# Optimization experiments

Measured on AMD Instinct MI355X. Metric: run time of the kernel, lower is better.

The kernel has to match this reference:

```python
import jax, jax.numpy as jnp
import numpy as np

NUM_NODES = 2048
NUM_OPS = 8
D, F, K = 64, 64, 64
H_NG = 128
H_EE = 64


def _make_edges(n):
    # edges[0]=i (src), edges[1]=j (dst) for i in [2,n), j in [0,i)
    src = np.concatenate([np.full(i, i, dtype=np.int64) for i in range(2, n)])
    dst = np.concatenate([np.arange(i, dtype=np.int64) for i in range(2, n)])
    return np.stack([src, dst])


def setup_inputs() -> dict:
    key = jax.random.key(0)
    ks = jax.random.split(key, 8)
    n = NUM_NODES
    s = lambda k, shape, fan_in: jax.random.normal(k, shape, jnp.float32) * (1.0 / np.sqrt(fan_in))
    return {
        "embed": jax.random.normal(ks[0], (n, D), jnp.float32),
        "W1": s(ks[1], (D, H_NG), D), "b1": jnp.zeros((H_NG,), jnp.float32),
        "W2": s(ks[2], (H_NG, H_NG), H_NG), "b2": jnp.zeros((H_NG,), jnp.float32),
        "W3": s(ks[3], (H_NG, F), H_NG), "b3": jnp.zeros((F,), jnp.float32),
        "We1": s(ks[4], (2 * F, H_EE), 2 * F), "be1": jnp.zeros((H_EE,), jnp.float32),
        "We2": s(ks[5], (H_EE, K), H_EE), "be2": jnp.zeros((K,), jnp.float32),
        "Wop": s(ks[6], (K, NUM_OPS), K), "bop": jnp.zeros((NUM_OPS,), jnp.float32),
        "edges": jnp.asarray(_make_edges(n)),
        "weights": jnp.ones((_make_edges(n).shape[1],), jnp.float32),
    }


def gcn_conv(x, W, b, src, dst, ew, n):
    # PyG GCNConv: x' = D^{-1/2} (A + I) D^{-1/2} (x W) + b, aggregated at dst
    h = x @ W
    loop = jnp.arange(n)
    src2 = jnp.concatenate([src, loop])
    dst2 = jnp.concatenate([dst, loop])
    w2 = jnp.concatenate([ew, jnp.ones((n,), x.dtype)])
    deg = jax.ops.segment_sum(w2, dst2, num_segments=n)
    dinv = jnp.where(deg > 0, jax.lax.rsqrt(deg), 0.0)
    norm = dinv[src2] * w2 * dinv[dst2]
    out = jax.ops.segment_sum(h[src2] * norm[:, None], dst2, num_segments=n)
    return out + b


def reference(embed, W1, b1, W2, b2, W3, b3, We1, be1, We2, be2, Wop, bop, edges, weights):
    n = embed.shape[0]
    src, dst = edges[0], edges[1]
    h = jax.nn.relu(gcn_conv(embed, W1, b1, src, dst, weights, n))
    h = jax.nn.relu(gcn_conv(h, W2, b2, src, dst, weights, n))
    h = jax.nn.relu(gcn_conv(h, W3, b3, src, dst, weights, n))  # [n, F]
    e = jnp.concatenate([h[src], h[dst]], axis=-1)              # [E, 2F]
    e = jax.nn.relu(e @ We1 + be1)
    e = jax.nn.relu(e @ We2 + be2)
    o = e @ Wop + bop                                            # [E, num_ops]
    p = jax.nn.softmax(o, axis=-1)
    # forward loop skips i == num_nodes-1; those rows of p remain zero
    mask = (src < n - 1)[:, None]
    return jnp.where(mask, p, 0.0)
```

## Files before the change

kernel.cpp:

```cpp
#include <hip/hip_runtime.h>
#include <math.h>

#define NN 2048
#define LASTN 2047

typedef __attribute__((ext_vector_type(8))) short short8;
typedef __attribute__((ext_vector_type(4))) float f32x4;
typedef __attribute__((ext_vector_type(4))) unsigned uint4v;

__device__ __forceinline__ float node_dinv(int j) {
  int deg = (j < 2) ? 2047 : (2048 - j);
  return rsqrtf((float)deg);
}

__device__ __forceinline__ void split_bf(float x, short& h, short& l) {
  unsigned u = __float_as_uint(x);
  unsigned r = u + 0x7FFFu + ((u >> 16) & 1u);
  h = (short)(r >> 16);
  float fh = __uint_as_float((r >> 16) << 16);
  float res = x - fh;
  unsigned u2 = __float_as_uint(res);
  unsigned r2 = u2 + 0x7FFFu + ((u2 >> 16) & 1u);
  l = (short)(r2 >> 16);
}

__device__ __forceinline__ unsigned cvt_pk_bf16(float a, float b) {
  unsigned r;
  asm("v_cvt_pk_bf16_f32 %0, %1, %2" : "=v"(r) : "v"(a), "v"(b));
  return r;
}

__device__ __forceinline__ void split_pair(float a, float b, unsigned& h, unsigned& l) {
  h = cvt_pk_bf16(a, b);
  float fa = __uint_as_float(h << 16);
  float fb = __uint_as_float(h & 0xFFFF0000u);
  l = cvt_pk_bf16(a - fa, b - fb);
}

__global__ __launch_bounds__(256) void prep(const float* __restrict__ embed,
                                            const float* __restrict__ We2,
                                            float* __restrict__ embedT,
                                            short* __restrict__ BfH,
                                            short* __restrict__ BfL) {
  __shared__ float tile[64][65];
  const int b = blockIdx.x;
  const int t = threadIdx.x;
  if (b < 32) {
    #pragma unroll
    for (int m = 0; m < 16; ++m) {
      int idx = m * 256 + t;
      int rl = idx >> 6, cc = idx & 63;
      tile[rl][cc] = embed[(b * 64 + rl) * 64 + cc];
    }
    __syncthreads();
    #pragma unroll
    for (int m = 0; m < 16; ++m) {
      int idx = m * 256 + t;
      int cc = idx >> 6, rl = idx & 63;
      embedT[cc * 2048 + b * 64 + rl] = tile[rl][cc];
    }
  } else {
    int tt = (b - 32) * 256 + t;
    int lane = tt & 63;
    int rest = tt >> 6;
    int ks = rest & 1;
    int ct = rest >> 1;
    int q = lane >> 4, l4 = lane & 15;
    int f = ct * 16 + l4;
    #pragma unroll
    for (int j = 0; j < 8; ++j) {
      int k = ks * 32 + q * 8 + j;
      float w = We2[k * 64 + f];
      short h, l;
      split_bf(w, h, l);
      int o = ((ct * 2 + ks) * 64 + lane) * 8 + j;
      BfH[o] = h;
      BfL[o] = l;
    }
  }
}

template <int K>
__global__ __launch_bounds__(512) void layer_fused(const float* __restrict__ XT,
                                                   const float* __restrict__ W,
                                                   const float* __restrict__ bias,
                                                   float* __restrict__ outT, int N) {
  const int c = blockIdx.x;
  const int t = threadIdx.x;
  __shared__ float wcol[K];
  __shared__ float sm[2048];
  __shared__ float part[512];
  if (t < K) wcol[t] = W[t * N + c];
  __syncthreads();
  float a0 = 0.f, a1 = 0.f, a2 = 0.f, a3 = 0.f;
  #pragma unroll 8
  for (int k = 0; k < K; ++k) {
    const float wk = wcol[k];
    const float* xr = XT + k * 2048 + t;
    a0 = fmaf(xr[0], wk, a0);
    a1 = fmaf(xr[512], wk, a1);
    a2 = fmaf(xr[1024], wk, a2);
    a3 = fmaf(xr[1536], wk, a3);
  }
  sm[t] = a0 * node_dinv(t);
  sm[t + 512] = a1 * node_dinv(t + 512);
  sm[t + 1024] = a2 * node_dinv(t + 1024);
  sm[t + 1536] = a3 * node_dinv(t + 1536);
  __syncthreads();
  const int j0 = 4 * t;
  float s0 = sm[j0], s1 = sm[j0 + 1], s2 = sm[j0 + 2], s3 = sm[j0 + 3];
  part[t] = (s0 + s1) + (s2 + s3);
  __syncthreads();
  for (int off = 1; off < 512; off <<= 1) {
    float v = part[t] + ((t + off < 512) ? part[t + off] : 0.f);
    __syncthreads();
    part[t] = v;
    __syncthreads();
  }
  float Q = (t < 511) ? part[t + 1] : 0.f;
  float Te3 = Q;
  float Te2 = Te3 + s3;
  float Te1 = Te2 + s2;
  float Te0 = Te1 + s1;
  const float bc = bias[c];
  float g0 = (j0 == 0) ? Te1 : Te0;
  float d0 = node_dinv(j0), d1 = node_dinv(j0 + 1);
  float d2 = node_dinv(j0 + 2), d3 = node_dinv(j0 + 3);
  float4 o;
  o.x = fmaxf(d0 * g0 + s0 * d0 + bc, 0.f);
  o.y = fmaxf(d1 * Te1 + s1 * d1 + bc, 0.f);
  o.z = fmaxf(d2 * Te2 + s2 * d2 + bc, 0.f);
  o.w = fmaxf(d3 * Te3 + s3 * d3 + bc, 0.f);
  *(float4*)(outT + (size_t)c * 2048 + j0) = o;
}

__global__ __launch_bounds__(256) void gemm_ab(const float* __restrict__ XT,
                                               const float* __restrict__ We1,
                                               const float* __restrict__ be1,
                                               float* __restrict__ A,
                                               float* __restrict__ B) {
  int idx = blockIdx.x * 256 + threadIdx.x;
  int r = idx >> 6, c = idx & 63;
  const float* WA = We1;
  const float* WB = We1 + 64 * 64;
  float a0 = 0.f, a1 = 0.f, b0 = 0.f, b1 = 0.f;
  for (int k = 0; k < 64; k += 2) {
    float x0 = XT[k * 2048 + r], x1 = XT[(k + 1) * 2048 + r];
    a0 = fmaf(x0, WA[k * 64 + c], a0);
    a1 = fmaf(x1, WA[(k + 1) * 64 + c], a1);
    b0 = fmaf(x0, WB[k * 64 + c], b0);
    b1 = fmaf(x1, WB[(k + 1) * 64 + c], b1);
  }
  A[idx] = a0 + a1 + be1[c];
  B[idx] = b0 + b1;
}

#define CHUNK 192
#define LSTR 196

__global__ __launch_bounds__(256, 3) void edge_mlp(const float* __restrict__ Amat,
                                                   const float* __restrict__ Bmat,
                                                   const short* __restrict__ BfH,
                                                   const short* __restrict__ BfL,
                                                   const float* __restrict__ be2,
                                                   const float* __restrict__ Wop,
                                                   const float* __restrict__ bop,
                                                   float* __restrict__ out) {
  const int i = LASTN - blockIdx.x;
  const long base = (long)i * (i - 1) / 2 - 1;
  const int tid = threadIdx.x;

  if (i == LASTN) {
    const float4 z = make_float4(0.f, 0.f, 0.f, 0.f);
    for (int j = blockIdx.y * 256 + tid; j < LASTN; j += gridDim.y * 256) {
      size_t off = ((size_t)(base + j)) * 8;
      *(float4*)(out + off) = z;
      *(float4*)(out + off + 4) = z;
    }
    return;
  }

  __shared__ __align__(16) float sm[64 * LSTR];

  const int l = tid & 63, w = tid >> 6;
  const int l4 = l & 15, q = l >> 4;

  const float4* Arow = (const float4*)(Amat + (size_t)i * 64);
  const float4 a00 = Arow[q * 2], a01 = Arow[q * 2 + 1];
  const float4 a10 = Arow[8 + q * 2], a11 = Arow[8 + q * 2 + 1];

  short8 Bh[8], Bl[8];
  #pragma unroll
  for (int u = 0; u < 8; ++u) {
    Bh[u] = *(const short8*)(BfH + (u * 64 + l) * 8);
    Bl[u] = *(const short8*)(BfL + (u * 64 + l) * 8);
  }

  #pragma unroll 1
  for (int cidx = blockIdx.y; cidx * CHUNK < i; cidx += gridDim.y) {
    const int j0 = cidx * CHUNK;

    #pragma unroll 1
    for (int mt = 0; mt < 3; ++mt) {
      const int mbase = (w * 3 + mt) * 16;
      int j = j0 + mbase + l4;
      int jc = min(j, i - 1);
      const float4* Brow = (const float4*)(Bmat + (size_t)jc * 64);

      short8 ah[2], al[2];
      #pragma unroll
      for (int ks = 0; ks < 2; ++ks) {
        float4 bb0 = Brow[ks * 8 + q * 2];
        float4 bb1 = Brow[ks * 8 + q * 2 + 1];
        float4 aa0 = ks ? a10 : a00;
        float4 aa1 = ks ? a11 : a01;
        float v0 = fmaxf(aa0.x + bb0.x, 0.f), v1 = fmaxf(aa0.y + bb0.y, 0.f);
        float v2 = fmaxf(aa0.z + bb0.z, 0.f), v3 = fmaxf(aa0.w + bb0.w, 0.f);
        float v4 = fmaxf(aa1.x + bb1.x, 0.f), v5 = fmaxf(aa1.y + bb1.y, 0.f);
        float v6 = fmaxf(aa1.z + bb1.z, 0.f), v7 = fmaxf(aa1.w + bb1.w, 0.f);
        unsigned h0, h1, h2, h3, L0, L1, L2, L3;
        split_pair(v0, v1, h0, L0);
        split_pair(v2, v3, h1, L1);
        split_pair(v4, v5, h2, L2);
        split_pair(v6, v7, h3, L3);
        ah[ks] = __builtin_bit_cast(short8, (uint4v){h0, h1, h2, h3});
        al[ks] = __builtin_bit_cast(short8, (uint4v){L0, L1, L2, L3});
      }

      f32x4 acc[4];
      #pragma unroll
      for (int ct = 0; ct < 4; ++ct) acc[ct] = (f32x4){0.f, 0.f, 0.f, 0.f};
      #pragma unroll
      for (int ct = 0; ct < 4; ++ct)
        acc[ct] = __builtin_amdgcn_mfma_f32_16x16x32_bf16(ah[0], Bh[ct * 2 + 0], acc[ct], 0, 0, 0);
      #pragma unroll
      for (int ct = 0; ct < 4; ++ct)
        acc[ct] = __builtin_amdgcn_mfma_f32_16x16x32_bf16(ah[1], Bh[ct * 2 + 1], acc[ct], 0, 0, 0);
      #pragma unroll
      for (int ct = 0; ct < 4; ++ct)
        acc[ct] = __builtin_amdgcn_mfma_f32_16x16x32_bf16(ah[0], Bl[ct * 2 + 0], acc[ct], 0, 0, 0);
      #pragma unroll
      for (int ct = 0; ct < 4; ++ct)
        acc[ct] = __builtin_amdgcn_mfma_f32_16x16x32_bf16(ah[1], Bl[ct * 2 + 1], acc[ct], 0, 0, 0);
      #pragma unroll
      for (int ct = 0; ct < 4; ++ct)
        acc[ct] = __builtin_amdgcn_mfma_f32_16x16x32_bf16(al[0], Bh[ct * 2 + 0], acc[ct], 0, 0, 0);
      #pragma unroll
      for (int ct = 0; ct < 4; ++ct)
        acc[ct] = __builtin_amdgcn_mfma_f32_16x16x32_bf16(al[1], Bh[ct * 2 + 1], acc[ct], 0, 0, 0);

      #pragma unroll
      for (int ct = 0; ct < 4; ++ct) {
        int f = ct * 16 + l4;
        float bias = be2[f];
        float4 st;
        st.x = fmaxf(acc[ct][0] + bias, 0.f);
        st.y = fmaxf(acc[ct][1] + bias, 0.f);
        st.z = fmaxf(acc[ct][2] + bias, 0.f);
        st.w = fmaxf(acc[ct][3] + bias, 0.f);
        *(float4*)(&sm[f * LSTR + mbase + q * 4]) = st;
      }
    }
    __syncthreads();

    if (tid < CHUNK) {
      int j = j0 + tid;
      if (j < i) {
        float o0 = bop[0], o1 = bop[1], o2 = bop[2], o3 = bop[3];
        float o4 = bop[4], o5 = bop[5], o6 = bop[6], o7 = bop[7];
        #pragma unroll 8
        for (int f = 0; f < 64; ++f) {
          float v = sm[f * LSTR + tid];
          o0 = fmaf(v, Wop[f * 8 + 0], o0);
          o1 = fmaf(v, Wop[f * 8 + 1], o1);
          o2 = fmaf(v, Wop[f * 8 + 2], o2);
          o3 = fmaf(v, Wop[f * 8 + 3], o3);
          o4 = fmaf(v, Wop[f * 8 + 4], o4);
          o5 = fmaf(v, Wop[f * 8 + 5], o5);
          o6 = fmaf(v, Wop[f * 8 + 6], o6);
          o7 = fmaf(v, Wop[f * 8 + 7], o7);
        }
        float mx = fmaxf(fmaxf(fmaxf(o0, o1), fmaxf(o2, o3)),
                         fmaxf(fmaxf(o4, o5), fmaxf(o6, o7)));
        float p0 = __expf(o0 - mx), p1 = __expf(o1 - mx), p2 = __expf(o2 - mx);
        float p3 = __expf(o3 - mx), p4 = __expf(o4 - mx), p5 = __expf(o5 - mx);
        float p6 = __expf(o6 - mx), p7 = __expf(o7 - mx);
        float rs = 1.0f / (((p0 + p1) + (p2 + p3)) + ((p4 + p5) + (p6 + p7)));
        size_t off = ((size_t)(base + j)) * 8;
        *(float4*)(out + off) = make_float4(p0 * rs, p1 * rs, p2 * rs, p3 * rs);
        *(float4*)(out + off + 4) = make_float4(p4 * rs, p5 * rs, p6 * rs, p7 * rs);
      }
    }
    __syncthreads();
  }
}

extern "C" void kernel_launch(void* const* d_in, const int* in_sizes, int n_in,
                              void* d_out, int out_size, void* d_ws, size_t ws_size,
                              hipStream_t stream) {
  const float* embed = (const float*)d_in[0];
  const float* W1 = (const float*)d_in[1];
  const float* b1 = (const float*)d_in[2];
  const float* W2 = (const float*)d_in[3];
  const float* b2 = (const float*)d_in[4];
  const float* W3 = (const float*)d_in[5];
  const float* b3 = (const float*)d_in[6];
  const float* We1 = (const float*)d_in[7];
  const float* be1 = (const float*)d_in[8];
  const float* We2 = (const float*)d_in[9];
  const float* be2 = (const float*)d_in[10];
  const float* Wop = (const float*)d_in[11];
  const float* bop = (const float*)d_in[12];

  float* ws = (float*)d_ws;
  float* embedT = ws;
  float* h2T = ws;
  float* h1T = ws + 262144;
  float* Abuf = ws + 262144;
  float* Bbuf = ws + 393216;
  float* h3T = ws + 524288;
  short* BfH = (short*)(ws + 655360);
  short* BfL = (short*)(ws + 657408);
  float* outp = (float*)d_out;

  prep<<<34, 256, 0, stream>>>(embed, We2, embedT, BfH, BfL);
  layer_fused<64><<<128, 512, 0, stream>>>(embedT, W1, b1, h1T, 128);
  layer_fused<128><<<128, 512, 0, stream>>>(h1T, W2, b2, h2T, 128);
  layer_fused<128><<<64, 512, 0, stream>>>(h2T, W3, b3, h3T, 64);
  gemm_ab<<<512, 256, 0, stream>>>(h3T, We1, be1, Abuf, Bbuf);

  dim3 ge(2046, 4, 1);
  edge_mlp<<<ge, 256, 0, stream>>>(Abuf, Bbuf, BfH, BfL, be2, Wop, bop, outp);
}
```

Measured before the change: 266.8 us.

## Double-buffer edge MLP chunks and overlap softmax epilogue with next MFMA stage

Shrinks the edge chunk to 64 rows and double-buffers the shared-memory hidden tile. One rotating wave runs the Wop projection and softmax on the current chunk while the other three waves compute the next chunk's MFMA tiles. This removes the phase where only some threads did the serial epilogue while the rest sat idle between barriers. It also halves the y-grid to 2, hoists the bias loads and raises the occupancy hint to 4. In exchange there are more barrier iterations per block and an uneven split of tiles across waves.

```diff
diff --git a/kernel.cpp b/kernel.cpp
--- a/kernel.cpp
+++ b/kernel.cpp
@@ -155,10 +155,11 @@
   B[idx] = b0 + b1;
 }
 
-#define CHUNK 192
-#define LSTR 196
-
-__global__ __launch_bounds__(256, 3) void edge_mlp(const float* __restrict__ Amat,
+#define CHUNK 64
+#define LSTR 68
+#define EGY 2
+
+__global__ __launch_bounds__(256, 4) void edge_mlp(const float* __restrict__ Amat,
                                                    const float* __restrict__ Bmat,
                                                    const short* __restrict__ BfH,
                                                    const short* __restrict__ BfL,
@@ -172,7 +173,7 @@
 
   if (i == LASTN) {
     const float4 z = make_float4(0.f, 0.f, 0.f, 0.f);
-    for (int j = blockIdx.y * 256 + tid; j < LASTN; j += gridDim.y * 256) {
+    for (int j = blockIdx.y * 256 + tid; j < LASTN; j += EGY * 256) {
       size_t off = ((size_t)(base + j)) * 8;
       *(float4*)(out + off) = z;
       *(float4*)(out + off + 4) = z;
@@ -180,7 +181,10 @@
     return;
   }
 
-  __shared__ __align__(16) float sm[64 * LSTR];
+  int c = blockIdx.y;
+  if (c * CHUNK >= i) return;
+
+  __shared__ __align__(16) float sm[2][64 * LSTR];
 
   const int l = tid & 63, w = tid >> 6;
   const int l4 = l & 15, q = l >> 4;
@@ -195,103 +199,122 @@
     Bh[u] = *(const short8*)(BfH + (u * 64 + l) * 8);
     Bl[u] = *(const short8*)(BfL + (u * 64 + l) * 8);
   }
-
-  #pragma unroll 1
-  for (int cidx = blockIdx.y; cidx * CHUNK < i; cidx += gridDim.y) {
-    const int j0 = cidx * CHUNK;
-
-    #pragma unroll 1
-    for (int mt = 0; mt < 3; ++mt) {
-      const int mbase = (w * 3 + mt) * 16;
-      int j = j0 + mbase + l4;
-      int jc = min(j, i - 1);
-      const float4* Brow = (const float4*)(Bmat + (size_t)jc * 64);
-
-      short8 ah[2], al[2];
-      #pragma unroll
-      for (int ks = 0; ks < 2; ++ks) {
-        float4 bb0 = Brow[ks * 8 + q * 2];
-        float4 bb1 = Brow[ks * 8 + q * 2 + 1];
-        float4 aa0 = ks ? a10 : a00;
-        float4 aa1 = ks ? a11 : a01;
-        float v0 = fmaxf(aa0.x + bb0.x, 0.f), v1 = fmaxf(aa0.y + bb0.y, 0.f);
-        float v2 = fmaxf(aa0.z + bb0.z, 0.f), v3 = fmaxf(aa0.w + bb0.w, 0.f);
-        float v4 = fmaxf(aa1.x + bb1.x, 0.f), v5 = fmaxf(aa1.y + bb1.y, 0.f);
-        float v6 = fmaxf(aa1.z + bb1.z, 0.f), v7 = fmaxf(aa1.w + bb1.w, 0.f);
-        unsigned h0, h1, h2, h3, L0, L1, L2, L3;
-        split_pair(v0, v1, h0, L0);
-        split_pair(v2, v3, h1, L1);
-        split_pair(v4, v5, h2, L2);
-        split_pair(v6, v7, h3, L3);
-        ah[ks] = __builtin_bit_cast(short8, (uint4v){h0, h1, h2, h3});
-        al[ks] = __builtin_bit_cast(short8, (uint4v){L0, L1, L2, L3});
+  float bias[4];
+  #pragma unroll
+  for (int ct = 0; ct < 4; ++ct) bias[ct] = be2[ct * 16 + l4];
+
+  auto stage_tile = [&](int cbase, int t, float* smb) {
+    int j = cbase + t * 16 + l4;
+    int jc = min(j, i - 1);
+    const float4* Brow = (const float4*)(Bmat + (size_t)jc * 64);
+
+    short8 ah[2], al[2];
+    #pragma unroll
+    for (int ks = 0; ks < 2; ++ks) {
+      float4 bb0 = Brow[ks * 8 + q * 2];
+      float4 bb1 = Brow[ks * 8 + q * 2 + 1];
+      float4 aa0 = ks ? a10 : a00;
+      float4 aa1 = ks ? a11 : a01;
+      float v0 = fmaxf(aa0.x + bb0.x, 0.f), v1 = fmaxf(aa0.y + bb0.y, 0.f);
+      float v2 = fmaxf(aa0.z + bb0.z, 0.f), v3 = fmaxf(aa0.w + bb0.w, 0.f);
+      float v4 = fmaxf(aa1.x + bb1.x, 0.f), v5 = fmaxf(aa1.y + bb1.y, 0.f);
+      float v6 = fmaxf(aa1.z + bb1.z, 0.f), v7 = fmaxf(aa1.w + bb1.w, 0.f);
+      unsigned h0, h1, h2, h3, L0, L1, L2, L3;
+      split_pair(v0, v1, h0, L0);
+      split_pair(v2, v3, h1, L1);
+      split_pair(v4, v5, h2, L2);
+      split_pair(v6, v7, h3, L3);
+      ah[ks] = __builtin_bit_cast(short8, (uint4v){h0, h1, h2, h3});
+      al[ks] = __builtin_bit_cast(short8, (uint4v){L0, L1, L2, L3});
+    }
+
+    f32x4 acc[4];
+    #pragma unroll
+    for (int ct = 0; ct < 4; ++ct) acc[ct] = (f32x4){0.f, 0.f, 0.f, 0.f};
+    #pragma unroll
+    for (int ct = 0; ct < 4; ++ct)
+      acc[ct] = __builtin_amdgcn_mfma_f32_16x16x32_bf16(ah[0], Bh[ct * 2 + 0], acc[ct], 0, 0, 0);
+    #pragma unroll
+    for (int ct = 0; ct < 4; ++ct)
+      acc[ct] = __builtin_amdgcn_mfma_f32_16x16x32_bf16(ah[1], Bh[ct * 2 + 1], acc[ct], 0, 0, 0);
+    #pragma unroll
+    for (int ct = 0; ct < 4; ++ct)
+      acc[ct] = __builtin_amdgcn_mfma_f32_16x16x32_bf16(ah[0], Bl[ct * 2 + 0], acc[ct], 0, 0, 0);
+    #pragma unroll
+    for (int ct = 0; ct < 4; ++ct)
+      acc[ct] = __builtin_amdgcn_mfma_f32_16x16x32_bf16(ah[1], Bl[ct * 2 + 1], acc[ct], 0, 0, 0);
+    #pragma unroll
+    for (int ct = 0; ct < 4; ++ct)
+      acc[ct] = __builtin_amdgcn_mfma_f32_16x16x32_bf16(al[0], Bh[ct * 2 + 0], acc[ct], 0, 0, 0);
+    #pragma unroll
+    for (int ct = 0; ct < 4; ++ct)
+      acc[ct] = __builtin_amdgcn_mfma_f32_16x16x32_bf16(al[1], Bh[ct * 2 + 1], acc[ct], 0, 0, 0);
+
+    #pragma unroll
+    for (int ct = 0; ct < 4; ++ct) {
+      int f = ct * 16 + l4;
+      float4 st;
+      st.x = fmaxf(acc[ct][0] + bias[ct], 0.f);
+      st.y = fmaxf(acc[ct][1] + bias[ct], 0.f);
+      st.z = fmaxf(acc[ct][2] + bias[ct], 0.f);
+      st.w = fmaxf(acc[ct][3] + bias[ct], 0.f);
+      *(float4*)(&smb[f * LSTR + t * 16 + q * 4]) = st;
+    }
+  };
+
+  auto phase_b = [&](int cbase, const float* smb) {
+    int j = cbase + l;
+    float o0 = bop[0], o1 = bop[1], o2 = bop[2], o3 = bop[3];
+    float o4 = bop[4], o5 = bop[5], o6 = bop[6], o7 = bop[7];
+    #pragma unroll 8
+    for (int f = 0; f < 64; ++f) {
+      float v = smb[f * LSTR + l];
+      o0 = fmaf(v, Wop[f * 8 + 0], o0);
+      o1 = fmaf(v, Wop[f * 8 + 1], o1);
+      o2 = fmaf(v, Wop[f * 8 + 2], o2);
+      o3 = fmaf(v, Wop[f * 8 + 3], o3);
+      o4 = fmaf(v, Wop[f * 8 + 4], o4);
+      o5 = fmaf(v, Wop[f * 8 + 5], o5);
+      o6 = fmaf(v, Wop[f * 8 + 6], o6);
+      o7 = fmaf(v, Wop[f * 8 + 7], o7);
+    }
+    float mx = fmaxf(fmaxf(fmaxf(o0, o1), fmaxf(o2, o3)),
+                     fmaxf(fmaxf(o4, o5), fmaxf(o6, o7)));
+    float p0 = __expf(o0 - mx), p1 = __expf(o1 - mx), p2 = __expf(o2 - mx);
+    float p3 = __expf(o3 - mx), p4 = __expf(o4 - mx), p5 = __expf(o5 - mx);
+    float p6 = __expf(o6 - mx), p7 = __expf(o7 - mx);
+    float rs = 1.0f / (((p0 + p1) + (p2 + p3)) + ((p4 + p5) + (p6 + p7)));
+    if (j < i) {
+      size_t off = ((size_t)(base + j)) * 8;
+      *(float4*)(out + off) = make_float4(p0 * rs, p1 * rs, p2 * rs, p3 * rs);
+      *(float4*)(out + off + 4) = make_float4(p4 * rs, p5 * rs, p6 * rs, p7 * rs);
+    }
+  };
+
+  stage_tile(c * CHUNK, w, sm[0]);
+  __syncthreads();
+
+  int buf = 0, kc = 0;
+  while (true) {
+    const int wb = kc & 3;
+    const int nc = c + EGY;
+    if (nc * CHUNK < i) {
+      int rel = (w - wb) & 3;
+      if (rel == 1) {
+        stage_tile(nc * CHUNK, 0, sm[buf ^ 1]);
+      } else if (rel == 2) {
+        stage_tile(nc * CHUNK, 1, sm[buf ^ 1]);
+        stage_tile(nc * CHUNK, 2, sm[buf ^ 1]);
+      } else if (rel == 3) {
+        stage_tile(nc * CHUNK, 3, sm[buf ^ 1]);
       }
-
-      f32x4 acc[4];
-      #pragma unroll
-      for (int ct = 0; ct < 4; ++ct) acc[ct] = (f32x4){0.f, 0.f, 0.f, 0.f};
-      #pragma unroll
-      for (int ct = 0; ct < 4; ++ct)
-        acc[ct] = __builtin_amdgcn_mfma_f32_16x16x32_bf16(ah[0], Bh[ct * 2 + 0], acc[ct], 0, 0, 0);
-      #pragma unroll
-      for (int ct = 0; ct < 4; ++ct)
-        acc[ct] = __builtin_amdgcn_mfma_f32_16x16x32_bf16(ah[1], Bh[ct * 2 + 1], acc[ct], 0, 0, 0);
-      #pragma unroll
-      for (int ct = 0; ct < 4; ++ct)
-        acc[ct] = __builtin_amdgcn_mfma_f32_16x16x32_bf16(ah[0], Bl[ct * 2 + 0], acc[ct], 0, 0, 0);
-      #pragma unroll
-      for (int ct = 0; ct < 4; ++ct)
-        acc[ct] = __builtin_amdgcn_mfma_f32_16x16x32_bf16(ah[1], Bl[ct * 2 + 1], acc[ct], 0, 0, 0);
-      #pragma unroll
-      for (int ct = 0; ct < 4; ++ct)
-        acc[ct] = __builtin_amdgcn_mfma_f32_16x16x32_bf16(al[0], Bh[ct * 2 + 0], acc[ct], 0, 0, 0);
-      #pragma unroll
-      for (int ct = 0; ct < 4; ++ct)
-        acc[ct] = __builtin_amdgcn_mfma_f32_16x16x32_bf16(al[1], Bh[ct * 2 + 1], acc[ct], 0, 0, 0);
-
-      #pragma unroll
-      for (int ct = 0; ct < 4; ++ct) {
-        int f = ct * 16 + l4;
-        float bias = be2[f];
-        float4 st;
-        st.x = fmaxf(acc[ct][0] + bias, 0.f);
-        st.y = fmaxf(acc[ct][1] + bias, 0.f);
-        st.z = fmaxf(acc[ct][2] + bias, 0.f);
-        st.w = fmaxf(acc[ct][3] + bias, 0.f);
-        *(float4*)(&sm[f * LSTR + mbase + q * 4]) = st;
-      }
-    }
+    }
+    if (w == wb) phase_b(c * CHUNK, sm[buf]);
     __syncthreads();
-
-    if (tid < CHUNK) {
-      int j = j0 + tid;
-      if (j < i) {
-        float o0 = bop[0], o1 = bop[1], o2 = bop[2], o3 = bop[3];
-        float o4 = bop[4], o5 = bop[5], o6 = bop[6], o7 = bop[7];
-        #pragma unroll 8
-        for (int f = 0; f < 64; ++f) {
-          float v = sm[f * LSTR + tid];
-          o0 = fmaf(v, Wop[f * 8 + 0], o0);
-          o1 = fmaf(v, Wop[f * 8 + 1], o1);
-          o2 = fmaf(v, Wop[f * 8 + 2], o2);
-          o3 = fmaf(v, Wop[f * 8 + 3], o3);
-          o4 = fmaf(v, Wop[f * 8 + 4], o4);
-          o5 = fmaf(v, Wop[f * 8 + 5], o5);
-          o6 = fmaf(v, Wop[f * 8 + 6], o6);
-          o7 = fmaf(v, Wop[f * 8 + 7], o7);
-        }
-        float mx = fmaxf(fmaxf(fmaxf(o0, o1), fmaxf(o2, o3)),
-                         fmaxf(fmaxf(o4, o5), fmaxf(o6, o7)));
-        float p0 = __expf(o0 - mx), p1 = __expf(o1 - mx), p2 = __expf(o2 - mx);
-        float p3 = __expf(o3 - mx), p4 = __expf(o4 - mx), p5 = __expf(o5 - mx);
-        float p6 = __expf(o6 - mx), p7 = __expf(o7 - mx);
-        float rs = 1.0f / (((p0 + p1) + (p2 + p3)) + ((p4 + p5) + (p6 + p7)));
-        size_t off = ((size_t)(base + j)) * 8;
-        *(float4*)(out + off) = make_float4(p0 * rs, p1 * rs, p2 * rs, p3 * rs);
-        *(float4*)(out + off + 4) = make_float4(p4 * rs, p5 * rs, p6 * rs, p7 * rs);
-      }
-    }
-    __syncthreads();
+    c = nc;
+    ++kc;
+    buf ^= 1;
+    if (c * CHUNK >= i) break;
   }
 }
 
@@ -329,6 +352,6 @@
   layer_fused<128><<<64, 512, 0, stream>>>(h2T, W3, b3, h3T, 64);
   gemm_ab<<<512, 256, 0, stream>>>(h3T, We1, be1, Abuf, Bbuf);
 
-  dim3 ge(2046, 4, 1);
+  dim3 ge(2046, EGY, 1);
   edge_mlp<<<ge, 256, 0, stream>>>(Abuf, Bbuf, BfH, BfL, be2, Wop, bop, outp);
 }
```

After: 254.3 us. 4.7% less time.

## Move edge output projection to MFMA with per-wave software pipelining

Applied to the files above, without the earlier changes.

Wop is pre-split into bf16 hi/lo fragments in prep, so the final 64->8 projection runs on MFMA (split-precision) instead of scalar FMAs over shared memory. The edge kernel is restructured so each wave owns its own 64-edge chunks with double-buffered, XOR-swizzled shared tiles. This removes the block-wide __syncthreads and overlaps stage-1 MFMA with the projection and softmax of the previous tile. Softmax now reduces across lanes with shuffles. In exchange, half the MFMA lanes carry padded zero columns and indexing gets more complex, with the MFMA operand order transposed.

```diff
diff --git a/kernel.cpp b/kernel.cpp
--- a/kernel.cpp
+++ b/kernel.cpp
@@ -39,9 +39,12 @@
 
 __global__ __launch_bounds__(256) void prep(const float* __restrict__ embed,
                                             const float* __restrict__ We2,
+                                            const float* __restrict__ Wop,
                                             float* __restrict__ embedT,
                                             short* __restrict__ BfH,
-                                            short* __restrict__ BfL) {
+                                            short* __restrict__ BfL,
+                                            short* __restrict__ WfH,
+                                            short* __restrict__ WfL) {
   __shared__ float tile[64][65];
   const int b = blockIdx.x;
   const int t = threadIdx.x;
@@ -59,7 +62,7 @@
       int cc = idx >> 6, rl = idx & 63;
       embedT[cc * 2048 + b * 64 + rl] = tile[rl][cc];
     }
-  } else {
+  } else if (b < 34) {
     int tt = (b - 32) * 256 + t;
     int lane = tt & 63;
     int rest = tt >> 6;
@@ -76,6 +79,20 @@
       int o = ((ct * 2 + ks) * 64 + lane) * 8 + j;
       BfH[o] = h;
       BfL[o] = l;
+    }
+  } else {
+    if (t < 128) {
+      int lane = t & 63, ks = t >> 6;
+      int q = lane >> 4, l4 = lane & 15;
+      #pragma unroll
+      for (int j = 0; j < 8; ++j) {
+        int k = ks * 32 + q * 8 + j;
+        float wv = (l4 < 8) ? Wop[k * 8 + l4] : 0.f;
+        short h, l;
+        split_bf(wv, h, l);
+        WfH[(ks * 64 + lane) * 8 + j] = h;
+        WfL[(ks * 64 + lane) * 8 + j] = l;
+      }
     }
   }
 }
@@ -155,15 +172,16 @@
   B[idx] = b0 + b1;
 }
 
-#define CHUNK 192
-#define LSTR 196
-
-__global__ __launch_bounds__(256, 3) void edge_mlp(const float* __restrict__ Amat,
+#define CHUNK 64
+#define EGY 4
+
+__global__ __launch_bounds__(128, 3) void edge_mlp(const float* __restrict__ Amat,
                                                    const float* __restrict__ Bmat,
                                                    const short* __restrict__ BfH,
                                                    const short* __restrict__ BfL,
+                                                   const short* __restrict__ WfH,
+                                                   const short* __restrict__ WfL,
                                                    const float* __restrict__ be2,
-                                                   const float* __restrict__ Wop,
                                                    const float* __restrict__ bop,
                                                    float* __restrict__ out) {
   const int i = LASTN - blockIdx.x;
@@ -172,7 +190,7 @@
 
   if (i == LASTN) {
     const float4 z = make_float4(0.f, 0.f, 0.f, 0.f);
-    for (int j = blockIdx.y * 256 + tid; j < LASTN; j += gridDim.y * 256) {
+    for (int j = blockIdx.y * 128 + tid; j < LASTN; j += EGY * 128) {
       size_t off = ((size_t)(base + j)) * 8;
       *(float4*)(out + off) = z;
       *(float4*)(out + off + 4) = z;
@@ -180,10 +198,15 @@
     return;
   }
 
-  __shared__ __align__(16) float sm[64 * LSTR];
-
   const int l = tid & 63, w = tid >> 6;
+  const int c0 = blockIdx.y * 2 + w;
+  if (c0 * CHUNK >= i) return;
+
+  __shared__ __align__(16) float sm[2][2][16 * 64];
+  float* smw = sm[w][0];
+
   const int l4 = l & 15, q = l >> 4;
+  const int wswz = (l4 & 7) << 2;
 
   const float4* Arow = (const float4*)(Amat + (size_t)i * 64);
   const float4 a00 = Arow[q * 2], a01 = Arow[q * 2 + 1];
@@ -195,103 +218,148 @@
     Bh[u] = *(const short8*)(BfH + (u * 64 + l) * 8);
     Bl[u] = *(const short8*)(BfL + (u * 64 + l) * 8);
   }
-
-  #pragma unroll 1
-  for (int cidx = blockIdx.y; cidx * CHUNK < i; cidx += gridDim.y) {
-    const int j0 = cidx * CHUNK;
-
-    #pragma unroll 1
-    for (int mt = 0; mt < 3; ++mt) {
-      const int mbase = (w * 3 + mt) * 16;
-      int j = j0 + mbase + l4;
-      int jc = min(j, i - 1);
-      const float4* Brow = (const float4*)(Bmat + (size_t)jc * 64);
-
-      short8 ah[2], al[2];
-      #pragma unroll
-      for (int ks = 0; ks < 2; ++ks) {
-        float4 bb0 = Brow[ks * 8 + q * 2];
-        float4 bb1 = Brow[ks * 8 + q * 2 + 1];
-        float4 aa0 = ks ? a10 : a00;
-        float4 aa1 = ks ? a11 : a01;
-        float v0 = fmaxf(aa0.x + bb0.x, 0.f), v1 = fmaxf(aa0.y + bb0.y, 0.f);
-        float v2 = fmaxf(aa0.z + bb0.z, 0.f), v3 = fmaxf(aa0.w + bb0.w, 0.f);
-        float v4 = fmaxf(aa1.x + bb1.x, 0.f), v5 = fmaxf(aa1.y + bb1.y, 0.f);
-        float v6 = fmaxf(aa1.z + bb1.z, 0.f), v7 = fmaxf(aa1.w + bb1.w, 0.f);
-        unsigned h0, h1, h2, h3, L0, L1, L2, L3;
-        split_pair(v0, v1, h0, L0);
-        split_pair(v2, v3, h1, L1);
-        split_pair(v4, v5, h2, L2);
-        split_pair(v6, v7, h3, L3);
-        ah[ks] = __builtin_bit_cast(short8, (uint4v){h0, h1, h2, h3});
-        al[ks] = __builtin_bit_cast(short8, (uint4v){L0, L1, L2, L3});
-      }
-
-      f32x4 acc[4];
-      #pragma unroll
-      for (int ct = 0; ct < 4; ++ct) acc[ct] = (f32x4){0.f, 0.f, 0.f, 0.f};
-      #pragma unroll
-      for (int ct = 0; ct < 4; ++ct)
-        acc[ct] = __builtin_amdgcn_mfma_f32_16x16x32_bf16(ah[0], Bh[ct * 2 + 0], acc[ct], 0, 0, 0);
-      #pragma unroll
-      for (int ct = 0; ct < 4; ++ct)
-        acc[ct] = __builtin_amdgcn_mfma_f32_16x16x32_bf16(ah[1], Bh[ct * 2 + 1], acc[ct], 0, 0, 0);
-      #pragma unroll
-      for (int ct = 0; ct < 4; ++ct)
-        acc[ct] = __builtin_amdgcn_mfma_f32_16x16x32_bf16(ah[0], Bl[ct * 2 + 0], acc[ct], 0, 0, 0);
-      #pragma unroll
-      for (int ct = 0; ct < 4; ++ct)
-        acc[ct] = __builtin_amdgcn_mfma_f32_16x16x32_bf16(ah[1], Bl[ct * 2 + 1], acc[ct], 0, 0, 0);
-      #pragma unroll
-      for (int ct = 0; ct < 4; ++ct)
-        acc[ct] = __builtin_amdgcn_mfma_f32_16x16x32_bf16(al[0], Bh[ct * 2 + 0], acc[ct], 0, 0, 0);
-      #pragma unroll
-      for (int ct = 0; ct < 4; ++ct)
-        acc[ct] = __builtin_amdgcn_mfma_f32_16x16x32_bf16(al[1], Bh[ct * 2 + 1], acc[ct], 0, 0, 0);
-
-      #pragma unroll
-      for (int ct = 0; ct < 4; ++ct) {
-        int f = ct * 16 + l4;
-        float bias = be2[f];
-        float4 st;
-        st.x = fmaxf(acc[ct][0] + bias, 0.f);
-        st.y = fmaxf(acc[ct][1] + bias, 0.f);
-        st.z = fmaxf(acc[ct][2] + bias, 0.f);
-        st.w = fmaxf(acc[ct][3] + bias, 0.f);
-        *(float4*)(&sm[f * LSTR + mbase + q * 4]) = st;
-      }
-    }
-    __syncthreads();
-
-    if (tid < CHUNK) {
-      int j = j0 + tid;
-      if (j < i) {
-        float o0 = bop[0], o1 = bop[1], o2 = bop[2], o3 = bop[3];
-        float o4 = bop[4], o5 = bop[5], o6 = bop[6], o7 = bop[7];
-        #pragma unroll 8
-        for (int f = 0; f < 64; ++f) {
-          float v = sm[f * LSTR + tid];
-          o0 = fmaf(v, Wop[f * 8 + 0], o0);
-          o1 = fmaf(v, Wop[f * 8 + 1], o1);
-          o2 = fmaf(v, Wop[f * 8 + 2], o2);
-          o3 = fmaf(v, Wop[f * 8 + 3], o3);
-          o4 = fmaf(v, Wop[f * 8 + 4], o4);
-          o5 = fmaf(v, Wop[f * 8 + 5], o5);
-          o6 = fmaf(v, Wop[f * 8 + 6], o6);
-          o7 = fmaf(v, Wop[f * 8 + 7], o7);
-        }
-        float mx = fmaxf(fmaxf(fmaxf(o0, o1), fmaxf(o2, o3)),
-                         fmaxf(fmaxf(o4, o5), fmaxf(o6, o7)));
-        float p0 = __expf(o0 - mx), p1 = __expf(o1 - mx), p2 = __expf(o2 - mx);
-        float p3 = __expf(o3 - mx), p4 = __expf(o4 - mx), p5 = __expf(o5 - mx);
-        float p6 = __expf(o6 - mx), p7 = __expf(o7 - mx);
-        float rs = 1.0f / (((p0 + p1) + (p2 + p3)) + ((p4 + p5) + (p6 + p7)));
-        size_t off = ((size_t)(base + j)) * 8;
-        *(float4*)(out + off) = make_float4(p0 * rs, p1 * rs, p2 * rs, p3 * rs);
-        *(float4*)(out + off + 4) = make_float4(p4 * rs, p5 * rs, p6 * rs, p7 * rs);
-      }
-    }
-    __syncthreads();
+  short8 Wh[2], Wl[2];
+  #pragma unroll
+  for (int s = 0; s < 2; ++s) {
+    Wh[s] = *(const short8*)(WfH + (s * 64 + l) * 8);
+    Wl[s] = *(const short8*)(WfL + (s * 64 + l) * 8);
+  }
+  float4 bias4[4];
+  #pragma unroll
+  for (int ct = 0; ct < 4; ++ct) bias4[ct] = ((const float4*)be2)[ct * 4 + q];
+  const float4 bopv = ((const float4*)bop)[q & 1];
+
+  auto STAGE = [&](int sc, int st, int sbuf) {
+    float* smb = smw + sbuf * 1024;
+    int j = sc * CHUNK + st * 16 + l4;
+    int jc = min(j, i - 1);
+    const float4* Brow = (const float4*)(Bmat + (size_t)jc * 64);
+    float4 g0 = Brow[q * 2], g1 = Brow[q * 2 + 1];
+    float4 g2 = Brow[8 + q * 2], g3 = Brow[8 + q * 2 + 1];
+
+    short8 ah[2], al[2];
+    #pragma unroll
+    for (int ks = 0; ks < 2; ++ks) {
+      float4 bb0 = ks ? g2 : g0;
+      float4 bb1 = ks ? g3 : g1;
+      float4 aa0 = ks ? a10 : a00;
+      float4 aa1 = ks ? a11 : a01;
+      float v0 = fmaxf(aa0.x + bb0.x, 0.f), v1 = fmaxf(aa0.y + bb0.y, 0.f);
+      float v2 = fmaxf(aa0.z + bb0.z, 0.f), v3 = fmaxf(aa0.w + bb0.w, 0.f);
+      float v4 = fmaxf(aa1.x + bb1.x, 0.f), v5 = fmaxf(aa1.y + bb1.y, 0.f);
+      float v6 = fmaxf(aa1.z + bb1.z, 0.f), v7 = fmaxf(aa1.w + bb1.w, 0.f);
+      unsigned h0, h1, h2, h3, L0, L1, L2, L3;
+      split_pair(v0, v1, h0, L0);
+      split_pair(v2, v3, h1, L1);
+      split_pair(v4, v5, h2, L2);
+      split_pair(v6, v7, h3, L3);
+      ah[ks] = __builtin_bit_cast(short8, (uint4v){h0, h1, h2, h3});
+      al[ks] = __builtin_bit_cast(short8, (uint4v){L0, L1, L2, L3});
+    }
+
+    f32x4 acc[4];
+    #pragma unroll
+    for (int ct = 0; ct < 4; ++ct) acc[ct] = (f32x4){0.f, 0.f, 0.f, 0.f};
+    #pragma unroll
+    for (int ct = 0; ct < 4; ++ct)
+      acc[ct] = __builtin_amdgcn_mfma_f32_16x16x32_bf16(Bh[ct * 2 + 0], ah[0], acc[ct], 0, 0, 0);
+    #pragma unroll
+    for (int ct = 0; ct < 4; ++ct)
+      acc[ct] = __builtin_amdgcn_mfma_f32_16x16x32_bf16(Bh[ct * 2 + 1], ah[1], acc[ct], 0, 0, 0);
+    #pragma unroll
+    for (int ct = 0; ct < 4; ++ct)
+      acc[ct] = __builtin_amdgcn_mfma_f32_16x16x32_bf16(Bl[ct * 2 + 0], ah[0], acc[ct], 0, 0, 0);
+    #pragma unroll
+    for (int ct = 0; ct < 4; ++ct)
+      acc[ct] = __builtin_amdgcn_mfma_f32_16x16x32_bf16(Bl[ct * 2 + 1], ah[1], acc[ct], 0, 0, 0);
+    #pragma unroll
+    for (int ct = 0; ct < 4; ++ct)
+      acc[ct] = __builtin_amdgcn_mfma_f32_16x16x32_bf16(Bh[ct * 2 + 0], al[0], acc[ct], 0, 0, 0);
+    #pragma unroll
+    for (int ct = 0; ct < 4; ++ct)
+      acc[ct] = __builtin_amdgcn_mfma_f32_16x16x32_bf16(Bh[ct * 2 + 1], al[1], acc[ct], 0, 0, 0);
+
+    #pragma unroll
+    for (int ct = 0; ct < 4; ++ct) {
+      float4 st4;
+      st4.x = fmaxf(acc[ct][0] + bias4[ct].x, 0.f);
+      st4.y = fmaxf(acc[ct][1] + bias4[ct].y, 0.f);
+      st4.z = fmaxf(acc[ct][2] + bias4[ct].z, 0.f);
+      st4.w = fmaxf(acc[ct][3] + bias4[ct].w, 0.f);
+      *(float4*)(&smb[l4 * 64 + ((ct * 16 + q * 4) ^ wswz)]) = st4;
+    }
+  };
+
+  auto FIN_READ = [&](int sbuf, float4& r0, float4& r1, float4& r2, float4& r3) {
+    const float* smb = smw + sbuf * 1024;
+    r0 = *(const float4*)(&smb[l4 * 64 + ((q * 8) ^ wswz)]);
+    r1 = *(const float4*)(&smb[l4 * 64 + ((q * 8 + 4) ^ wswz)]);
+    r2 = *(const float4*)(&smb[l4 * 64 + ((32 + q * 8) ^ wswz)]);
+    r3 = *(const float4*)(&smb[l4 * 64 + ((32 + q * 8 + 4) ^ wswz)]);
+  };
+
+  auto FIN_REST = [&](int sc, int st, float4 r0, float4 r1, float4 r2, float4 r3) {
+    unsigned h0, h1, h2, h3, L0, L1, L2, L3;
+    split_pair(r0.x, r0.y, h0, L0);
+    split_pair(r0.z, r0.w, h1, L1);
+    split_pair(r1.x, r1.y, h2, L2);
+    split_pair(r1.z, r1.w, h3, L3);
+    short8 Eh0 = __builtin_bit_cast(short8, (uint4v){h0, h1, h2, h3});
+    short8 El0 = __builtin_bit_cast(short8, (uint4v){L0, L1, L2, L3});
+    split_pair(r2.x, r2.y, h0, L0);
+    split_pair(r2.z, r2.w, h1, L1);
+    split_pair(r3.x, r3.y, h2, L2);
+    split_pair(r3.z, r3.w, h3, L3);
+    short8 Eh1 = __builtin_bit_cast(short8, (uint4v){h0, h1, h2, h3});
+    short8 El1 = __builtin_bit_cast(short8, (uint4v){L0, L1, L2, L3});
+
+    f32x4 acc2 = (f32x4){0.f, 0.f, 0.f, 0.f};
+    acc2 = __builtin_amdgcn_mfma_f32_16x16x32_bf16(Wh[0], Eh0, acc2, 0, 0, 0);
+    acc2 = __builtin_amdgcn_mfma_f32_16x16x32_bf16(Wh[1], Eh1, acc2, 0, 0, 0);
+    acc2 = __builtin_amdgcn_mfma_f32_16x16x32_bf16(Wh[0], El0, acc2, 0, 0, 0);
+    acc2 = __builtin_amdgcn_mfma_f32_16x16x32_bf16(Wh[1], El1, acc2, 0, 0, 0);
+    acc2 = __builtin_amdgcn_mfma_f32_16x16x32_bf16(Wl[0], Eh0, acc2, 0, 0, 0);
+    acc2 = __builtin_amdgcn_mfma_f32_16x16x32_bf16(Wl[1], Eh1, acc2, 0, 0, 0);
+    acc2 = __builtin_amdgcn_mfma_f32_16x16x32_bf16(Wl[0], El0, acc2, 0, 0, 0);
+    acc2 = __builtin_amdgcn_mfma_f32_16x16x32_bf16(Wl[1], El1, acc2, 0, 0, 0);
+
+    float v0 = acc2[0] + bopv.x, v1 = acc2[1] + bopv.y;
+    float v2 = acc2[2] + bopv.z, v3 = acc2[3] + bopv.w;
+    float u0 = __shfl_xor(v0, 16), u1 = __shfl_xor(v1, 16);
+    float u2 = __shfl_xor(v2, 16), u3 = __shfl_xor(v3, 16);
+    float mx = fmaxf(fmaxf(fmaxf(v0, v1), fmaxf(v2, v3)),
+                     fmaxf(fmaxf(u0, u1), fmaxf(u2, u3)));
+    float pv0 = __expf(v0 - mx), pv1 = __expf(v1 - mx);
+    float pv2 = __expf(v2 - mx), pv3 = __expf(v3 - mx);
+    float pu0 = __expf(u0 - mx), pu1 = __expf(u1 - mx);
+    float pu2 = __expf(u2 - mx), pu3 = __expf(u3 - mx);
+    float sv = (pv0 + pv1) + (pv2 + pv3);
+    float su = (pu0 + pu1) + (pu2 + pu3);
+    float rs = 1.0f / (sv + su);
+    int j = sc * CHUNK + st * 16 + l4;
+    if (q < 2 && j < i) {
+      *(float4*)(out + ((size_t)(base + j)) * 8 + q * 4) =
+          make_float4(pv0 * rs, pv1 * rs, pv2 * rs, pv3 * rs);
+    }
+  };
+
+  int cc = c0, tt = 1;
+  int fc = c0, ft = 0;
+  int fbuf = 0;
+  STAGE(c0, 0, 0);
+  while (true) {
+    if (tt == 4) { tt = 0; cc += 2 * EGY; }
+    float4 r0, r1, r2, r3;
+    FIN_READ(fbuf, r0, r1, r2, r3);
+    if (cc * CHUNK < i) {
+      STAGE(cc, tt, fbuf ^ 1);
+      FIN_REST(fc, ft, r0, r1, r2, r3);
+      fc = cc; ft = tt; fbuf ^= 1;
+      ++tt;
+    } else {
+      FIN_REST(fc, ft, r0, r1, r2, r3);
+      break;
+    }
   }
 }
 
@@ -321,14 +389,16 @@
   float* h3T = ws + 524288;
   short* BfH = (short*)(ws + 655360);
   short* BfL = (short*)(ws + 657408);
+  short* WfH = (short*)(ws + 659456);
+  short* WfL = (short*)(ws + 659968);
   float* outp = (float*)d_out;
 
-  prep<<<34, 256, 0, stream>>>(embed, We2, embedT, BfH, BfL);
+  prep<<<35, 256, 0, stream>>>(embed, We2, Wop, embedT, BfH, BfL, WfH, WfL);
   layer_fused<64><<<128, 512, 0, stream>>>(embedT, W1, b1, h1T, 128);
   layer_fused<128><<<128, 512, 0, stream>>>(h1T, W2, b2, h2T, 128);
   layer_fused<128><<<64, 512, 0, stream>>>(h2T, W3, b3, h3T, 64);
   gemm_ab<<<512, 256, 0, stream>>>(h3T, We1, be1, Abuf, Bbuf);
 
-  dim3 ge(2046, 4, 1);
-  edge_mlp<<<ge, 256, 0, stream>>>(Abuf, Bbuf, BfH, BfL, be2, Wop, bop, outp);
-}
+  dim3 ge(2046, EGY, 1);
+  edge_mlp<<<ge, 128, 0, stream>>>(Abuf, Bbuf, BfH, BfL, WfH, WfL, be2, bop, outp);
+}
```

Measured after the change: 325.4 us. 22.0% more time.
